# Kernel tuning notes

Measured on AMD Instinct MI355X. Metric: run time of the kernel, lower is better.

Reference implementation:

```python
import jax, jax.numpy as jnp
import numpy as np

D_MODEL = 1024
NUM_HEADS = 16
D_K = D_MODEL // NUM_HEADS
D_MLP = 4096
EPS = 1e-5


def setup_inputs() -> dict:
    key = jax.random.key(0)
    ks = jax.random.split(key, 16)
    s = 0.02
    inp = {
        "x": jax.random.normal(ks[0], (2, 2048, D_MODEL), dtype=jnp.float32),
        "Wq": jax.random.normal(ks[1], (D_MODEL, D_MODEL), dtype=jnp.float32) * s,
        "bq": jnp.zeros((D_MODEL,), jnp.float32),
        "Wk": jax.random.normal(ks[2], (D_MODEL, D_MODEL), dtype=jnp.float32) * s,
        "bk": jnp.zeros((D_MODEL,), jnp.float32),
        "Wv": jax.random.normal(ks[3], (D_MODEL, D_MODEL), dtype=jnp.float32) * s,
        "bv": jnp.zeros((D_MODEL,), jnp.float32),
        "Wo": jax.random.normal(ks[4], (D_MODEL, D_MODEL), dtype=jnp.float32) * s,
        "bo": jnp.zeros((D_MODEL,), jnp.float32),
        "W1": jax.random.normal(ks[5], (D_MODEL, D_MLP), dtype=jnp.float32) * s,
        "b1": jnp.zeros((D_MLP,), jnp.float32),
        "W2": jax.random.normal(ks[6], (D_MLP, D_MODEL), dtype=jnp.float32) * s,
        "b2": jnp.zeros((D_MODEL,), jnp.float32),
        "ln1_g": jnp.ones((D_MODEL,), jnp.float32),
        "ln1_b": jnp.zeros((D_MODEL,), jnp.float32),
        "ln2_g": jnp.ones((D_MODEL,), jnp.float32),
        "ln2_b": jnp.zeros((D_MODEL,), jnp.float32),
    }
    return inp


def _layer_norm(x, g, b):
    mu = jnp.mean(x, axis=-1, keepdims=True)
    var = jnp.var(x, axis=-1, keepdims=True)
    return (x - mu) * jax.lax.rsqrt(var + EPS) * g + b


def _split_heads(x):
    b, s, _ = x.shape
    return x.reshape(b, s, NUM_HEADS, D_K).transpose(0, 2, 1, 3)  # [b,h,s,dk]


def reference(x, Wq, bq, Wk, bk, Wv, bv, Wo, bo, W1, b1, W2, b2,
              ln1_g, ln1_b, ln2_g, ln2_b):
    b, s, _ = x.shape
    q = _split_heads(x @ Wq + bq)
    k = _split_heads(x @ Wk + bk)
    v = _split_heads(x @ Wv + bv)
    # [b,h,s,s] scores, scaled by sqrt(d_k) as in the original
    score = jnp.einsum("bhqd,bhkd->bhqk", q, k) / jnp.sqrt(jnp.float32(D_K))
    attn = jax.nn.softmax(score, axis=-1)
    out = jnp.einsum("bhqk,bhkd->bhqd", attn, v)
    out = out.transpose(0, 2, 1, 3).reshape(b, s, D_MODEL)
    out = out @ Wo + bo
    # residual + norm1 (dropout is identity in eval)
    x = _layer_norm(x + out, ln1_g, ln1_b)
    # feed-forward
    h = jax.nn.relu(x @ W1 + b1)
    ff = h @ W2 + b2
    x = _layer_norm(x + ff, ln2_g, ln2_b)
    return x
```

## Files before the change

### kernel.cpp

```cpp
#include <hip/hip_runtime.h>
#include <hip/hip_bf16.h>
#include <cstdint>

#define DEV __device__ __forceinline__

typedef __attribute__((ext_vector_type(8))) __bf16 bf16x8;
typedef __attribute__((ext_vector_type(4))) float f32x4;

DEV uint16_t f2b(float f) {
  __hip_bfloat16 h = __float2bfloat16(f);
  return *(uint16_t*)&h;
}
DEV uint32_t pkbf2(float a, float b) {
  return (uint32_t)f2b(a) | ((uint32_t)f2b(b) << 16);
}
DEV uint64_t pkbf4(float a, float b, float c, float d) {
  return (uint64_t)pkbf2(a, b) | ((uint64_t)pkbf2(c, d) << 32);
}

DEV void gload_lds16(const void* g, void* l) {
  __builtin_amdgcn_global_load_lds(
      (const __attribute__((address_space(1))) void*)g,
      (__attribute__((address_space(3))) void*)l, 16, 0, 0);
}

DEV bf16x8 scale8(bf16x8 v, float sc) {
  union { bf16x8 b; uint16_t u[8]; } in, out;
  in.b = v;
#pragma unroll
  for (int i = 0; i < 8; i++) {
    float x = __uint_as_float(((uint32_t)in.u[i]) << 16);
    out.u[i] = f2b(x * sc);
  }
  return out.b;
}

__global__ __launch_bounds__(256) void prep_all(
    const float* __restrict__ x, uint16_t* __restrict__ xb,
    const float* __restrict__ Wq, const float* __restrict__ Wk,
    const float* __restrict__ Wv, uint16_t* __restrict__ wqkt,
    const float* __restrict__ Wo, uint16_t* __restrict__ wot,
    const float* __restrict__ W1, uint16_t* __restrict__ w1t,
    const float* __restrict__ W2, uint16_t* __restrict__ w2t,
    const float* __restrict__ bq, const float* __restrict__ bk,
    const float* __restrict__ bv, float* __restrict__ bqkv) {
  __shared__ float t[32][33];
  int bid = blockIdx.x, tid = threadIdx.x;
  if (bid < 4096) {
    int i = bid * 256 + tid;
    float4 v = ((const float4*)x)[i];
    ((uint64_t*)xb)[i] = pkbf4(v.x, v.y, v.z, v.w);
    return;
  }
  if (bid >= 16384) {
    int i = (bid - 16384) * 256 + tid;
    if (i < 3072)
      bqkv[i] = i < 1024 ? bq[i] : (i < 2048 ? bk[i - 1024] : bv[i - 2048]);
    return;
  }
  const float* src;
  uint16_t* dst;
  int R, C, bx, by;
  if (bid < 8192) {
    int local = bid - 4096;
    if (local < 3072) {
      int z = local >> 10, rem = local & 1023;
      src = z == 0 ? Wq : (z == 1 ? Wk : Wv);
      dst = wqkt + (size_t)z * 1024 * 1024;
      R = 1024; C = 1024; bx = rem & 31; by = rem >> 5;
    } else {
      int rem = local - 3072;
      src = Wo; dst = wot; R = 1024; C = 1024; bx = rem & 31; by = rem >> 5;
    }
  } else if (bid < 12288) {
    int rem = bid - 8192;
    src = W1; dst = w1t; R = 1024; C = 4096; bx = rem & 127; by = rem >> 7;
  } else {
    int rem = bid - 12288;
    src = W2; dst = w2t; R = 4096; C = 1024; bx = rem & 31; by = rem >> 5;
  }
  int c0 = bx * 32, r0 = by * 32;
  int lrow = tid >> 3, lc = (tid & 7) * 4;
  float4 v = *(const float4*)&src[(size_t)(r0 + lrow) * C + c0 + lc];
  t[lrow][lc] = v.x; t[lrow][lc + 1] = v.y;
  t[lrow][lc + 2] = v.z; t[lrow][lc + 3] = v.w;
  __syncthreads();
  int cr = tid >> 3, rq = (tid & 7) * 4;
  uint64_t r = pkbf4(t[rq][cr], t[rq + 1][cr], t[rq + 2][cr], t[rq + 3][cr]);
  *(uint64_t*)&dst[(size_t)(c0 + cr) * R + r0 + rq] = r;
}

template <int MODE, int NSPLIT, int BK, int QKV>
__global__ __launch_bounds__(256) void gemm_bt(
    const uint16_t* __restrict__ A, const uint16_t* __restrict__ Bt,
    const float* __restrict__ bias, void* __restrict__ Cv,
    uint16_t* __restrict__ vt, int M, int N, int K, int nx) {
  __shared__ uint16_t As[2][128 * BK];
  __shared__ uint16_t Bs[2][128 * BK];
  int nwg = gridDim.x, bid = blockIdx.x;
  int cpx = nwg >> 3;
  int swzb = (bid & 7) * cpx + (bid >> 3);
  int ntile = nwg / NSPLIT;
  int sp = swzb / ntile, r = swzb % ntile;
  int n0 = (r % nx) * 128, m0 = (r / nx) * 128;
  int Klen = K / NSPLIT;
  int tid = threadIdx.x, w = tid >> 6, l = tid & 63;
  int wr = w >> 1, wc = w & 1;
  int lr = l & 15, lg = l >> 4, lk8 = lg * 8;
  f32x4 acc[4][4] = {};
  const uint16_t* Ab = A + (size_t)m0 * K + sp * Klen;
  const uint16_t* Bb = Bt + (size_t)n0 * K + sp * Klen;

  auto stage = [&](int buf, int k0) {
    if (BK == 32) {
#pragma unroll
      for (int i = 0; i < 2; i++) {
        int c = 2 * w + i;
        int rr = c * 16 + (l >> 2);
        gload_lds16(Ab + (size_t)rr * K + k0 + (l & 3) * 8, &As[buf][c * 512]);
        gload_lds16(Bb + (size_t)rr * K + k0 + (l & 3) * 8, &Bs[buf][c * 512]);
      }
    } else {
      int colb = (((l & 7) ^ ((l >> 3) & 7)) << 4);
#pragma unroll
      for (int i = 0; i < 4; i++) {
        int c = 4 * w + i;
        int rr = c * 8 + (l >> 3);
        gload_lds16((const uint8_t*)(Ab + (size_t)rr * K + k0) + colb,
                    &As[buf][c * 512]);
        gload_lds16((const uint8_t*)(Bb + (size_t)rr * K + k0) + colb,
                    &Bs[buf][c * 512]);
      }
    }
  };

  stage(0, 0);
  __syncthreads();

  for (int k0 = 0; k0 < Klen; k0 += BK) {
    int cur = (k0 / BK) & 1;
    if (k0 + BK < Klen) stage(cur ^ 1, k0 + BK);
    if (BK == 32) {
      bf16x8 af[4], bf[4];
#pragma unroll
      for (int m = 0; m < 4; m++)
        af[m] = *(const bf16x8*)&As[cur][(wr * 64 + m * 16 + lr) * 32 + lk8];
#pragma unroll
      for (int n = 0; n < 4; n++)
        bf[n] = *(const bf16x8*)&Bs[cur][(wc * 64 + n * 16 + lr) * 32 + lk8];
#pragma unroll
      for (int m = 0; m < 4; m++)
#pragma unroll
        for (int n = 0; n < 4; n++)
          acc[m][n] = __builtin_amdgcn_mfma_f32_16x16x32_bf16(af[m], bf[n], acc[m][n], 0, 0, 0);
    } else {
      int sw = (lr & 7) << 4;
#pragma unroll
      for (int ks = 0; ks < 2; ks++) {
        int off = ((ks << 6) | (lg << 4)) ^ sw;
        bf16x8 af[4], bf[4];
#pragma unroll
        for (int m = 0; m < 4; m++)
          af[m] = *(const bf16x8*)((const uint8_t*)&As[cur][(wr * 64 + m * 16 + lr) * 64] + off);
#pragma unroll
        for (int n = 0; n < 4; n++)
          bf[n] = *(const bf16x8*)((const uint8_t*)&Bs[cur][(wc * 64 + n * 16 + lr) * 64] + off);
#pragma unroll
        for (int m = 0; m < 4; m++)
#pragma unroll
          for (int n = 0; n < 4; n++)
            acc[m][n] = __builtin_amdgcn_mfma_f32_16x16x32_bf16(af[m], bf[n], acc[m][n], 0, 0, 0);
      }
    }
    __syncthreads();
  }

  int g4 = lg * 4;
  if (QKV && n0 >= 2048) {
#pragma unroll
    for (int m = 0; m < 4; m++) {
      int row = m0 + wr * 64 + m * 16 + g4;
      int b_ = row >> 11, s_ = row & 2047;
#pragma unroll
      for (int n = 0; n < 4; n++) {
        int c = n0 - 2048 + wc * 64 + n * 16 + lr;
        float bv = bias[n0 + wc * 64 + n * 16 + lr];
        uint64_t pk = pkbf4(acc[m][n][0] + bv, acc[m][n][1] + bv,
                            acc[m][n][2] + bv, acc[m][n][3] + bv);
        size_t vidx = ((size_t)(b_ * 16 + (c >> 6))) * 131072 +
                      (size_t)(c & 63) * 2048 + s_;
        *(uint64_t*)&vt[vidx] = pk;
      }
    }
    return;
  }
#pragma unroll
  for (int m = 0; m < 4; m++) {
    int row = m0 + wr * 64 + m * 16 + g4;
#pragma unroll
    for (int n = 0; n < 4; n++) {
      int col = n0 + wc * 64 + n * 16 + lr;
      float bv = (NSPLIT == 1 || sp == 0) ? bias[col] : 0.f;
#pragma unroll
      for (int j = 0; j < 4; j++) {
        float v = acc[m][n][j] + bv;
        if (MODE == 2) v = fmaxf(v, 0.f);
        size_t idx = (size_t)sp * M * N + (size_t)(row + j) * N + col;
        if (MODE == 0) ((float*)Cv)[idx] = v;
        else           ((uint16_t*)Cv)[idx] = f2b(v);
      }
    }
  }
}

template <int MODE, int NSPLIT>
__global__ __launch_bounds__(512, 2) void gemm256(
    const uint16_t* __restrict__ A, const uint16_t* __restrict__ Bt,
    const float* __restrict__ bias, void* __restrict__ Cv,
    int M, int N, int K, int nx) {
  __shared__ uint16_t As[2][256 * 64];
  __shared__ uint16_t Bs[2][256 * 64];
  int nwg = gridDim.x, bid = blockIdx.x;
  int cpx = nwg >> 3;
  int swzb = (bid & 7) * cpx + (bid >> 3);
  int ntile = nwg / NSPLIT;
  int sp = swzb / ntile, rr0 = swzb % ntile;
  int n0 = (rr0 % nx) * 256, m0 = (rr0 / nx) * 256;
  int Klen = K / NSPLIT;
  int tid = threadIdx.x, w = tid >> 6, l = tid & 63;
  int wr = w >> 2, wc = w & 3;
  int lr = l & 15, lg = l >> 4;
  f32x4 acc[8][4] = {};
  const uint16_t* Ab = A + (size_t)m0 * K + sp * Klen;
  const uint16_t* Bb = Bt + (size_t)n0 * K + sp * Klen;
  int colb = (((l & 7) ^ (l >> 3)) << 4);
  int srl = l >> 3;

  auto stageH = [&](int buf, int k0, int h) {
    const uint16_t* base = (h < 2) ? Ab : Bb;
    uint16_t* lds = (h < 2) ? &As[buf][0] : &Bs[buf][0];
    int hh = (h & 1) * 128;
#pragma unroll
    for (int j = 0; j < 2; j++) {
      int rr = hh + j * 64 + w * 8;
      gload_lds16((const uint8_t*)(base + (size_t)(rr + srl) * K + k0) + colb,
                  &lds[rr * 64]);
    }
  };

#pragma unroll
  for (int h = 0; h < 4; h++) stageH(0, 0, h);
  asm volatile("s_waitcnt vmcnt(0)" ::: "memory");
  __builtin_amdgcn_s_barrier();

  int nt = Klen >> 6;
  int swr = (lr & 7) << 4;
  for (int t = 0; t < nt; t++) {
    int buf = t & 1;
    bf16x8 bfr[2][4];
#pragma unroll
    for (int ks = 0; ks < 2; ks++) {
#pragma unroll
      for (int mq = 0; mq < 2; mq++) {
        const int ph = ks * 2 + mq;
        int off = ((ks << 6) | (lg << 4)) ^ swr;
        bf16x8 af[4];
#pragma unroll
        for (int m = 0; m < 4; m++) {
          int row = wr * 128 + (mq * 4 + m) * 16 + lr;
          af[m] = *(const bf16x8*)((const uint8_t*)&As[buf][row * 64] + off);
        }
        if (mq == 0) {
#pragma unroll
          for (int n = 0; n < 4; n++) {
            int row = wc * 64 + n * 16 + lr;
            bfr[ks][n] = *(const bf16x8*)((const uint8_t*)&Bs[buf][row * 64] + off);
          }
        }
        if (t + 1 < nt) {
          if (ph == 0) { stageH(buf ^ 1, (t + 1) * 64, 0); stageH(buf ^ 1, (t + 1) * 64, 1); }
          if (ph == 1) { stageH(buf ^ 1, (t + 1) * 64, 2); stageH(buf ^ 1, (t + 1) * 64, 3); }
        }
        __builtin_amdgcn_s_barrier();
        asm volatile("s_waitcnt lgkmcnt(0)" ::: "memory");
        __builtin_amdgcn_sched_barrier(0);
        __builtin_amdgcn_s_setprio(1);
#pragma unroll
        for (int m = 0; m < 4; m++)
#pragma unroll
          for (int n = 0; n < 4; n++)
            acc[mq * 4 + m][n] = __builtin_amdgcn_mfma_f32_16x16x32_bf16(
                af[m], bfr[ks][n], acc[mq * 4 + m][n], 0, 0, 0);
        __builtin_amdgcn_s_setprio(0);
        if (ph == 3) asm volatile("s_waitcnt vmcnt(0)" ::: "memory");
        __builtin_amdgcn_s_barrier();
      }
    }
  }

#pragma unroll
  for (int m = 0; m < 8; m++) {
    int row = m0 + wr * 128 + m * 16 + lg * 4;
#pragma unroll
    for (int n = 0; n < 4; n++) {
      int col = n0 + wc * 64 + n * 16 + lr;
      float bv = (NSPLIT == 1 || sp == 0) ? bias[col] : 0.f;
#pragma unroll
      for (int j = 0; j < 4; j++) {
        float v = acc[m][n][j] + bv;
        if (MODE == 2) v = fmaxf(v, 0.f);
        size_t idx = (size_t)sp * M * N + (size_t)(row + j) * N + col;
        if (MODE == 0) ((float*)Cv)[idx] = v;
        else           ((uint16_t*)Cv)[idx] = f2b(v);
      }
    }
  }
}

__global__ __launch_bounds__(256, 2) void attn_fused(
    const uint16_t* __restrict__ qkv, const uint16_t* __restrict__ Vt,
    uint16_t* __restrict__ outb) {
  constexpr int LQ = 3072;
  constexpr float SC = 0.18033688f;
  int L = blockIdx.x;
  int qb = (L >> 3) & 15;
  int bh = (L & 7) + 8 * (L >> 7);
  int b = bh >> 4, h = bh & 15;
  int w = threadIdx.x >> 6, l = threadIdx.x & 63;
  int lr = l & 15, lg = l >> 4;
  int qbase = qb * 128 + w * 32;

  __shared__ uint16_t Kbuf[2][2][64 * 64];
  __shared__ uint16_t Vbuf[2][2][64 * 64];
  __shared__ uint16_t Plds[4][2][16 * 64];
  uint16_t* PwA = &Plds[w][0][0];
  uint16_t* PwB = &Plds[w][1][0];

  const uint16_t* qrowA = qkv + (size_t)(b * 2048 + qbase + lr) * LQ + h * 64;
  const uint16_t* qrowB = qrowA + (size_t)16 * LQ;
  bf16x8 qA0 = scale8(*(const bf16x8*)(qrowA + lg * 8), SC);
  bf16x8 qA1 = scale8(*(const bf16x8*)(qrowA + 32 + lg * 8), SC);
  bf16x8 qB0 = scale8(*(const bf16x8*)(qrowB + lg * 8), SC);
  bf16x8 qB1 = scale8(*(const bf16x8*)(qrowB + 32 + lg * 8), SC);

  float rsA = 0.f, rsB = 0.f;
  f32x4 oA[4] = {}, oB[4] = {};

  const uint8_t* kq = (const uint8_t*)qkv;
  const uint8_t* vq = (const uint8_t*)Vt;
  int colb = (((l & 7) ^ ((l >> 3) & 7)) << 4);
  int Rl = w * 16 + (l >> 3);

  auto stageKV = [&](int buf, int kb) {
#pragma unroll
    for (int s2 = 0; s2 < 2; s2++) {
#pragma unroll
      for (int c2 = 0; c2 < 2; c2++) {
        int R = Rl + c2 * 8;
        const uint8_t* ks =
            kq + ((size_t)(b * 2048 + kb + s2 * 64 + R) * LQ + 1024 + h * 64) * 2 + colb;
        gload_lds16(ks, &Kbuf[buf][s2][(w * 16 + c2 * 8) * 64]);
        const uint8_t* vs =
            vq + ((size_t)(bh * 64 + R) * 2048 + kb + s2 * 64) * 2 + colb;
        gload_lds16(vs, &Vbuf[buf][s2][(w * 16 + c2 * 8) * 64]);
      }
    }
  };

  stageKV(0, 0);
  __syncthreads();

  int swz = (lr & 7) << 4;
  for (int kb = 0; kb < 2048; kb += 128) {
    int cur = (kb >> 7) & 1;
    if (kb + 128 < 2048) stageKV(cur ^ 1, kb + 128);

#pragma unroll
    for (int s2 = 0; s2 < 2; s2++) {
      const uint8_t* Kb = (const uint8_t*)Kbuf[cur][s2];
      const uint8_t* Vb = (const uint8_t*)Vbuf[cur][s2];
      f32x4 sA[4], sB[4];
      __builtin_amdgcn_s_setprio(1);
#pragma unroll
      for (int t = 0; t < 4; t++) {
        const uint8_t* rb = Kb + (16 * t + lr) * 128;
        bf16x8 k0 = *(const bf16x8*)(rb + ((lg << 4) ^ swz));
        bf16x8 k1 = *(const bf16x8*)(rb + ((64 | (lg << 4)) ^ swz));
        f32x4 zA = {};
        zA = __builtin_amdgcn_mfma_f32_16x16x32_bf16(k0, qA0, zA, 0, 0, 0);
        zA = __builtin_amdgcn_mfma_f32_16x16x32_bf16(k1, qA1, zA, 0, 0, 0);
        sA[t] = zA;
        f32x4 zB = {};
        zB = __builtin_amdgcn_mfma_f32_16x16x32_bf16(k0, qB0, zB, 0, 0, 0);
        zB = __builtin_amdgcn_mfma_f32_16x16x32_bf16(k1, qB1, zB, 0, 0, 0);
        sB[t] = zB;
      }
      __builtin_amdgcn_s_setprio(0);
#pragma unroll
      for (int t = 0; t < 4; t++) {
        float a0 = __builtin_amdgcn_exp2f(sA[t][0]);
        float a1 = __builtin_amdgcn_exp2f(sA[t][1]);
        float a2 = __builtin_amdgcn_exp2f(sA[t][2]);
        float a3 = __builtin_amdgcn_exp2f(sA[t][3]);
        rsA += (a0 + a1) + (a2 + a3);
        uint2 pa;
        pa.x = pkbf2(a0, a1);
        pa.y = pkbf2(a2, a3);
        *(uint2*)((uint8_t*)PwA + lr * 128 + ((t * 32 + lg * 8) ^ swz)) = pa;
        float b0 = __builtin_amdgcn_exp2f(sB[t][0]);
        float b1 = __builtin_amdgcn_exp2f(sB[t][1]);
        float b2 = __builtin_amdgcn_exp2f(sB[t][2]);
        float b3 = __builtin_amdgcn_exp2f(sB[t][3]);
        rsB += (b0 + b1) + (b2 + b3);
        uint2 pb;
        pb.x = pkbf2(b0, b1);
        pb.y = pkbf2(b2, b3);
        *(uint2*)((uint8_t*)PwB + lr * 128 + ((t * 32 + lg * 8) ^ swz)) = pb;
      }
      __builtin_amdgcn_wave_barrier();
      bf16x8 pA0 = *(const bf16x8*)((const uint8_t*)PwA + lr * 128 + ((lg << 4) ^ swz));
      bf16x8 pA1 = *(const bf16x8*)((const uint8_t*)PwA + lr * 128 + ((64 | (lg << 4)) ^ swz));
      bf16x8 pB0 = *(const bf16x8*)((const uint8_t*)PwB + lr * 128 + ((lg << 4) ^ swz));
      bf16x8 pB1 = *(const bf16x8*)((const uint8_t*)PwB + lr * 128 + ((64 | (lg << 4)) ^ swz));
      __builtin_amdgcn_s_setprio(1);
#pragma unroll
      for (int t = 0; t < 4; t++) {
        const uint8_t* rb = Vb + (16 * t + lr) * 128;
        bf16x8 v0 = *(const bf16x8*)(rb + ((lg << 4) ^ swz));
        bf16x8 v1 = *(const bf16x8*)(rb + ((64 | (lg << 4)) ^ swz));
        oA[t] = __builtin_amdgcn_mfma_f32_16x16x32_bf16(v0, pA0, oA[t], 0, 0, 0);
        oA[t] = __builtin_amdgcn_mfma_f32_16x16x32_bf16(v1, pA1, oA[t], 0, 0, 0);
        oB[t] = __builtin_amdgcn_mfma_f32_16x16x32_bf16(v0, pB0, oB[t], 0, 0, 0);
        oB[t] = __builtin_amdgcn_mfma_f32_16x16x32_bf16(v1, pB1, oB[t], 0, 0, 0);
      }
      __builtin_amdgcn_s_setprio(0);
      if (s2 == 0) __builtin_amdgcn_wave_barrier();
    }
    __syncthreads();
  }
  rsA += __shfl_xor(rsA, 16);
  rsA += __shfl_xor(rsA, 32);
  rsB += __shfl_xor(rsB, 16);
  rsB += __shfl_xor(rsB, 32);
  float invA = 1.f / rsA, invB = 1.f / rsB;
  uint16_t* orowA = outb + (size_t)(b * 2048 + qbase + lr) * 1024 + h * 64;
  uint16_t* orowB = orowA + (size_t)16 * 1024;
#pragma unroll
  for (int t = 0; t < 4; t++) {
    uint2 ra;
    ra.x = pkbf2(oA[t][0] * invA, oA[t][1] * invA);
    ra.y = pkbf2(oA[t][2] * invA, oA[t][3] * invA);
    *(uint2*)(orowA + t * 16 + lg * 4) = ra;
    uint2 rb2;
    rb2.x = pkbf2(oB[t][0] * invB, oB[t][1] * invB);
    rb2.y = pkbf2(oB[t][2] * invB, oB[t][3] * invB);
    *(uint2*)(orowB + t * 16 + lg * 4) = rb2;
  }
}

template <int XBF, int WF32, int WB16, int NPART>
__global__ __launch_bounds__(256) void ln_res(
    const void* __restrict__ xr, const uint16_t* __restrict__ parts,
    const float* __restrict__ gam, const float* __restrict__ bet,
    float* __restrict__ of32, uint16_t* __restrict__ ob16) {
  int row = blockIdx.x, t = threadIdx.x;
  int w = t >> 6, l = t & 63;
  float v0, v1, v2, v3;
  if (XBF) {
    uint2 u = ((const uint2*)((const uint16_t*)xr + (size_t)row * 1024))[t];
    v0 = __uint_as_float((u.x & 0xffffu) << 16);
    v1 = __uint_as_float(u.x & 0xffff0000u);
    v2 = __uint_as_float((u.y & 0xffffu) << 16);
    v3 = __uint_as_float(u.y & 0xffff0000u);
  } else {
    float4 xv = ((const float4*)((const float*)xr + (size_t)row * 1024))[t];
    v0 = xv.x; v1 = xv.y; v2 = xv.z; v3 = xv.w;
  }
#pragma unroll
  for (int p = 0; p < NPART; p++) {
    uint2 u = ((const uint2*)(parts + (size_t)p * 4096 * 1024 +
                              (size_t)row * 1024))[t];
    v0 += __uint_as_float((u.x & 0xffffu) << 16);
    v1 += __uint_as_float(u.x & 0xffff0000u);
    v2 += __uint_as_float((u.y & 0xffffu) << 16);
    v3 += __uint_as_float(u.y & 0xffff0000u);
  }
  float s = v0 + v1 + v2 + v3;
  float sq = v0 * v0 + v1 * v1 + v2 * v2 + v3 * v3;
#pragma unroll
  for (int d = 1; d < 64; d <<= 1) {
    s += __shfl_xor(s, d);
    sq += __shfl_xor(sq, d);
  }
  __shared__ float red[8];
  if (l == 0) { red[w] = s; red[4 + w] = sq; }
  __syncthreads();
  s = red[0] + red[1] + red[2] + red[3];
  sq = red[4] + red[5] + red[6] + red[7];
  float mean = s * (1.f / 1024.f);
  float var = sq * (1.f / 1024.f) - mean * mean;
  float rstd = rsqrtf(var + 1e-5f);
  float4 gv = ((const float4*)gam)[t];
  float4 bv = ((const float4*)bet)[t];
  float y0 = (v0 - mean) * rstd * gv.x + bv.x;
  float y1 = (v1 - mean) * rstd * gv.y + bv.y;
  float y2 = (v2 - mean) * rstd * gv.z + bv.z;
  float y3 = (v3 - mean) * rstd * gv.w + bv.w;
  if (WF32) {
    float4 yv; yv.x = y0; yv.y = y1; yv.z = y2; yv.w = y3;
    ((float4*)(of32 + (size_t)row * 1024))[t] = yv;
  }
  if (WB16) {
    uint2 r;
    r.x = pkbf2(y0, y1);
    r.y = pkbf2(y2, y3);
    ((uint2*)(ob16 + (size_t)row * 1024))[t] = r;
  }
}

static constexpr size_t OFF_XB    = 0;
static constexpr size_t OFF_WQKVT = (size_t)8 << 20;
static constexpr size_t OFF_WOT   = (size_t)14 << 20;
static constexpr size_t OFF_W1T   = (size_t)16 << 20;
static constexpr size_t OFF_W2T   = (size_t)24 << 20;
static constexpr size_t OFF_BIAS  = (size_t)32 << 20;
static constexpr size_t OFF_QKV   = OFF_BIAS + ((size_t)64 << 10);
static constexpr size_t OFF_VT    = OFF_QKV + ((size_t)24 << 20);
static constexpr size_t OFF_PROJ  = OFF_VT + ((size_t)8 << 20);
static constexpr size_t OFF_LN1B  = OFF_PROJ + ((size_t)32 << 20);
static constexpr size_t OFF_ATTN  = OFF_LN1B + ((size_t)8 << 20);

extern "C" void kernel_launch(void* const* d_in, const int* in_sizes, int n_in,
                              void* d_out, int out_size, void* d_ws, size_t ws_size,
                              hipStream_t stream) {
  const float* x   = (const float*)d_in[0];
  const float* Wq  = (const float*)d_in[1];
  const float* bq  = (const float*)d_in[2];
  const float* Wk  = (const float*)d_in[3];
  const float* bk  = (const float*)d_in[4];
  const float* Wv  = (const float*)d_in[5];
  const float* bv  = (const float*)d_in[6];
  const float* Wo  = (const float*)d_in[7];
  const float* bo  = (const float*)d_in[8];
  const float* W1  = (const float*)d_in[9];
  const float* b1  = (const float*)d_in[10];
  const float* W2  = (const float*)d_in[11];
  const float* b2  = (const float*)d_in[12];
  const float* g1  = (const float*)d_in[13];
  const float* be1 = (const float*)d_in[14];
  const float* g2  = (const float*)d_in[15];
  const float* be2 = (const float*)d_in[16];
  float* out = (float*)d_out;
  uint8_t* ws = (uint8_t*)d_ws;

  uint16_t* xb    = (uint16_t*)(ws + OFF_XB);
  uint16_t* wqkt  = (uint16_t*)(ws + OFF_WQKVT);
  uint16_t* wot   = (uint16_t*)(ws + OFF_WOT);
  uint16_t* w1t   = (uint16_t*)(ws + OFF_W1T);
  uint16_t* w2t   = (uint16_t*)(ws + OFF_W2T);
  float*    bqkv  = (float*)(ws + OFF_BIAS);
  uint16_t* qkvb  = (uint16_t*)(ws + OFF_QKV);
  uint16_t* vt    = (uint16_t*)(ws + OFF_VT);
  uint16_t* proj  = (uint16_t*)(ws + OFF_PROJ);
  uint16_t* ln1b  = (uint16_t*)(ws + OFF_LN1B);
  uint16_t* attnb = (uint16_t*)(ws + OFF_ATTN);
  uint16_t* hbuf  = (uint16_t*)(ws + OFF_QKV);

  prep_all<<<16396, 256, 0, stream>>>(x, xb, Wq, Wk, Wv, wqkt, Wo, wot,
                                      W1, w1t, W2, w2t, bq, bk, bv, bqkv);
  gemm_bt<1, 1, 32, 1><<<768, 256, 0, stream>>>(xb, wqkt, bqkv, qkvb, vt,
                                                4096, 3072, 1024, 24);
  attn_fused<<<512, 256, 0, stream>>>(qkvb, vt, attnb);
  gemm_bt<1, 2, 64, 0><<<512, 256, 0, stream>>>(attnb, wot, bo, proj, nullptr,
                                                4096, 1024, 1024, 8);
  ln_res<1, 0, 1, 2><<<4096, 256, 0, stream>>>(xb, proj, g1, be1,
                                               nullptr, ln1b);
  gemm256<2, 1><<<256, 512, 0, stream>>>(ln1b, w1t, b1, hbuf,
                                         4096, 4096, 1024, 16);
  gemm256<1, 4><<<256, 512, 0, stream>>>(hbuf, w2t, b2, proj,
                                         4096, 1024, 4096, 4);
  ln_res<1, 1, 0, 4><<<4096, 256, 0, stream>>>(ln1b, proj, g2, be2,
                                               out, nullptr);
}
```

Measured before the change: 207.1 us.

## Add triple-buffered QKV GEMM kernel with fine-grained waitcnt and setprio

Splits the QKV projection out of the generic gemm_bt into a dedicated kernel that uses three LDS buffers and prefetches two k-steps ahead. Explicit vmcnt waits replace full syncs, and s_setprio raises wave priority around the MFMA block. The aim is to hide global-to-LDS load latency better in the first GEMM. It costs more LDS per block, which may reduce occupancy, and uses hand-tuned wait counts that depend on the per-stage load count.

Result: slower. 225.6 us (+9.0%).

```diff
diff --git a/kernel.cpp b/kernel.cpp
--- a/kernel.cpp
+++ b/kernel.cpp
@@ -90,11 +90,11 @@
   *(uint64_t*)&dst[(size_t)(c0 + cr) * R + r0 + rq] = r;
 }
 
-template <int MODE, int NSPLIT, int BK, int QKV>
+template <int MODE, int NSPLIT, int BK>
 __global__ __launch_bounds__(256) void gemm_bt(
     const uint16_t* __restrict__ A, const uint16_t* __restrict__ Bt,
     const float* __restrict__ bias, void* __restrict__ Cv,
-    uint16_t* __restrict__ vt, int M, int N, int K, int nx) {
+    int M, int N, int K, int nx) {
   __shared__ uint16_t As[2][128 * BK];
   __shared__ uint16_t Bs[2][128 * BK];
   int nwg = gridDim.x, bid = blockIdx.x;
@@ -176,7 +176,83 @@
   }
 
   int g4 = lg * 4;
-  if (QKV && n0 >= 2048) {
+#pragma unroll
+  for (int m = 0; m < 4; m++) {
+    int row = m0 + wr * 64 + m * 16 + g4;
+#pragma unroll
+    for (int n = 0; n < 4; n++) {
+      int col = n0 + wc * 64 + n * 16 + lr;
+      float bv = (NSPLIT == 1 || sp == 0) ? bias[col] : 0.f;
+#pragma unroll
+      for (int j = 0; j < 4; j++) {
+        float v = acc[m][n][j] + bv;
+        if (MODE == 2) v = fmaxf(v, 0.f);
+        size_t idx = (size_t)sp * M * N + (size_t)(row + j) * N + col;
+        if (MODE == 0) ((float*)Cv)[idx] = v;
+        else           ((uint16_t*)Cv)[idx] = f2b(v);
+      }
+    }
+  }
+}
+
+__global__ __launch_bounds__(256) void gemm_qkv_r3(
+    const uint16_t* __restrict__ A, const uint16_t* __restrict__ Bt,
+    const float* __restrict__ bias, uint16_t* __restrict__ Cv,
+    uint16_t* __restrict__ vt, int M, int N, int K, int nx) {
+  __shared__ uint16_t As[3][128 * 32];
+  __shared__ uint16_t Bs[3][128 * 32];
+  int nwg = gridDim.x, bid = blockIdx.x;
+  int cpx = nwg >> 3;
+  int swzb = (bid & 7) * cpx + (bid >> 3);
+  int n0 = (swzb % nx) * 128, m0 = (swzb / nx) * 128;
+  int tid = threadIdx.x, w = tid >> 6, l = tid & 63;
+  int wr = w >> 1, wc = w & 1;
+  int lr = l & 15, lg = l >> 4, lk8 = lg * 8;
+  f32x4 acc[4][4] = {};
+  const uint16_t* Ab = A + (size_t)m0 * K;
+  const uint16_t* Bb = Bt + (size_t)n0 * K;
+
+  auto stage = [&](int buf, int k0) {
+#pragma unroll
+    for (int i = 0; i < 2; i++) {
+      int c = 2 * w + i;
+      int rr = c * 16 + (l >> 2);
+      gload_lds16(Ab + (size_t)rr * K + k0 + (l & 3) * 8, &As[buf][c * 512]);
+      gload_lds16(Bb + (size_t)rr * K + k0 + (l & 3) * 8, &Bs[buf][c * 512]);
+    }
+  };
+
+  int ns = K >> 5;
+  stage(0, 0);
+  stage(1, 32);
+  for (int s = 0; s < ns; s++) {
+    int cur = s % 3;
+    if (s + 2 < ns) stage((s + 2) % 3, (s + 2) * 32);
+    if (s + 2 < ns)      asm volatile("s_waitcnt vmcnt(8)" ::: "memory");
+    else if (s + 1 < ns) asm volatile("s_waitcnt vmcnt(4)" ::: "memory");
+    else                 asm volatile("s_waitcnt vmcnt(0)" ::: "memory");
+    __builtin_amdgcn_s_barrier();
+    bf16x8 af[4], bf[4];
+#pragma unroll
+    for (int m = 0; m < 4; m++)
+      af[m] = *(const bf16x8*)&As[cur][(wr * 64 + m * 16 + lr) * 32 + lk8];
+#pragma unroll
+    for (int n = 0; n < 4; n++)
+      bf[n] = *(const bf16x8*)&Bs[cur][(wc * 64 + n * 16 + lr) * 32 + lk8];
+    asm volatile("s_waitcnt lgkmcnt(0)" ::: "memory");
+    __builtin_amdgcn_sched_barrier(0);
+    __builtin_amdgcn_s_setprio(1);
+#pragma unroll
+    for (int m = 0; m < 4; m++)
+#pragma unroll
+      for (int n = 0; n < 4; n++)
+        acc[m][n] = __builtin_amdgcn_mfma_f32_16x16x32_bf16(af[m], bf[n], acc[m][n], 0, 0, 0);
+    __builtin_amdgcn_s_setprio(0);
+    __builtin_amdgcn_s_barrier();
+  }
+
+  int g4 = lg * 4;
+  if (n0 >= 2048) {
 #pragma unroll
     for (int m = 0; m < 4; m++) {
       int row = m0 + wr * 64 + m * 16 + g4;
@@ -200,15 +276,10 @@
 #pragma unroll
     for (int n = 0; n < 4; n++) {
       int col = n0 + wc * 64 + n * 16 + lr;
-      float bv = (NSPLIT == 1 || sp == 0) ? bias[col] : 0.f;
-#pragma unroll
-      for (int j = 0; j < 4; j++) {
-        float v = acc[m][n][j] + bv;
-        if (MODE == 2) v = fmaxf(v, 0.f);
-        size_t idx = (size_t)sp * M * N + (size_t)(row + j) * N + col;
-        if (MODE == 0) ((float*)Cv)[idx] = v;
-        else           ((uint16_t*)Cv)[idx] = f2b(v);
-      }
+      float bv = bias[col];
+#pragma unroll
+      for (int j = 0; j < 4; j++)
+        Cv[(size_t)(row + j) * N + col] = f2b(acc[m][n][j] + bv);
     }
   }
 }
@@ -568,11 +639,11 @@
 
   prep_all<<<16396, 256, 0, stream>>>(x, xb, Wq, Wk, Wv, wqkt, Wo, wot,
                                       W1, w1t, W2, w2t, bq, bk, bv, bqkv);
-  gemm_bt<1, 1, 32, 1><<<768, 256, 0, stream>>>(xb, wqkt, bqkv, qkvb, vt,
-                                                4096, 3072, 1024, 24);
+  gemm_qkv_r3<<<768, 256, 0, stream>>>(xb, wqkt, bqkv, qkvb, vt,
+                                       4096, 3072, 1024, 24);
   attn_fused<<<512, 256, 0, stream>>>(qkvb, vt, attnb);
-  gemm_bt<1, 2, 64, 0><<<512, 256, 0, stream>>>(attnb, wot, bo, proj, nullptr,
-                                                4096, 1024, 1024, 8);
+  gemm_bt<1, 2, 64><<<512, 256, 0, stream>>>(attnb, wot, bo, proj,
+                                             4096, 1024, 1024, 8);
   ln_res<1, 0, 1, 2><<<4096, 256, 0, stream>>>(xb, proj, g1, be1,
                                                nullptr, ln1b);
   gemm256<2, 1><<<256, 512, 0, stream>>>(ln1b, w1t, b1, hbuf,
```
